# Performance work log

Hardware: AMD Instinct MI355X
Metric: run time of the kernel (lower is better)

The kernel has to match this reference:

```python
import jax, jax.numpy as jnp
import numpy as np

B, N, C = 2, 2048, 1024
H, D = 16, 64          # num_heads, head_dim
FF = 4096              # mlp hidden = 4*C
EPS = 1e-5


def layernorm(x, g, b):
    mu = jnp.mean(x, axis=-1, keepdims=True)
    var = jnp.mean((x - mu) ** 2, axis=-1, keepdims=True)
    return (x - mu) * jax.lax.rsqrt(var + EPS) * g + b


def setup_inputs() -> dict:
    key = jax.random.key(0)
    ks = jax.random.split(key, 8)
    s = lambda d: 1.0 / np.sqrt(d)
    return {
        "x": jax.random.normal(ks[0], (B, N, C), jnp.float32),
        "ln1_g": jnp.ones((C,), jnp.float32),
        "ln1_b": jnp.zeros((C,), jnp.float32),
        "qkv_w": jax.random.normal(ks[1], (3 * C, C), jnp.float32) * s(C),
        "proj_w": jax.random.normal(ks[2], (C, C), jnp.float32) * s(C),
        "proj_b": jnp.zeros((C,), jnp.float32),
        "ln2_g": jnp.ones((C,), jnp.float32),
        "ln2_b": jnp.zeros((C,), jnp.float32),
        "w1": jax.random.normal(ks[3], (FF, C), jnp.float32) * s(C),
        "b1": jnp.zeros((FF,), jnp.float32),
        "w2": jax.random.normal(ks[4], (C, FF), jnp.float32) * s(FF),
        "b2": jnp.zeros((C,), jnp.float32),
    }


def reference(x, ln1_g, ln1_b, qkv_w, proj_w, proj_b, ln2_g, ln2_b, w1, b1, w2, b2):
    # ---- attention sub-block ----
    h = layernorm(x, ln1_g, ln1_b)                       # [B,N,C]
    qkv = h @ qkv_w.T                                    # [B,N,3C]
    qkv = qkv.reshape(B, N, 3, H, D).transpose(2, 0, 3, 1, 4)  # [3,B,H,N,D]
    q, k, v = qkv[0], qkv[1], qkv[2]
    scale = D ** -0.5
    attn = jnp.einsum("bhnd,bhmd->bhnm", q, k) * scale   # [B,H,N,N]
    attn = jax.nn.softmax(attn, axis=-1)
    ao = jnp.einsum("bhnm,bhmd->bhnd", attn, v)          # [B,H,N,D]
    ao = ao.transpose(0, 2, 1, 3).reshape(B, N, C)
    x = x + ao @ proj_w.T + proj_b
    # ---- MLP sub-block ----
    h2 = layernorm(x, ln2_g, ln2_b)
    mlp = jax.nn.gelu(h2 @ w1.T + b1, approximate=False) @ w2.T + b2
    return x + mlp
```

## Files before the change

### kernel.cpp

```cpp
#include <hip/hip_runtime.h>
#include <hip/hip_bf16.h>

typedef __hip_bfloat16 obf;
typedef __attribute__((ext_vector_type(8))) __bf16 bf16x8;
typedef __attribute__((ext_vector_type(4))) float f32x4;

#define DEVINL __device__ __forceinline__

DEVINL void gload_lds16(const void* g, void* l) {
  __builtin_amdgcn_global_load_lds((const __attribute__((address_space(1))) void*)g,
                                   (__attribute__((address_space(3))) void*)l,
                                   16, 0, 0);
}

__global__ void __launch_bounds__(256) f2b_kernel(const float* __restrict__ in,
                                                  __bf16* __restrict__ out, int n8)
{
  const int i = blockIdx.x * 256 + threadIdx.x;
  if (i >= n8) return;
  const float4 a = ((const float4*)in)[i * 2];
  const float4 b = ((const float4*)in)[i * 2 + 1];
  bf16x8 o;
  o[0] = (__bf16)a.x; o[1] = (__bf16)a.y; o[2] = (__bf16)a.z; o[3] = (__bf16)a.w;
  o[4] = (__bf16)b.x; o[5] = (__bf16)b.y; o[6] = (__bf16)b.z; o[7] = (__bf16)b.w;
  ((bf16x8*)out)[i] = o;
}

__global__ void __launch_bounds__(256) ln_f2b2_kernel(
    const float* __restrict__ xin, const float* __restrict__ g, const float* __restrict__ b,
    obf* __restrict__ lnout,
    const float* __restrict__ win1, __bf16* __restrict__ wout1, int n8_1, int nb1,
    const float* __restrict__ win2, __bf16* __restrict__ wout2, int n8_2,
    int nln)
{
  __shared__ float red[8];
  const int t = threadIdx.x;
  const int bx = blockIdx.x;
  if (bx < nln) {
    const int row = bx;
    const int lane = t & 63, w = t >> 6;
    float4 f = ((const float4*)xin)[(size_t)row * 256 + t];
    float v[4] = { f.x, f.y, f.z, f.w };
    float s1 = v[0] + v[1] + v[2] + v[3];
    float s2 = v[0]*v[0] + v[1]*v[1] + v[2]*v[2] + v[3]*v[3];
    #pragma unroll
    for (int off = 32; off >= 1; off >>= 1) {
      s1 += __shfl_xor(s1, off);
      s2 += __shfl_xor(s2, off);
    }
    if (lane == 0) { red[w] = s1; red[4 + w] = s2; }
    __syncthreads();
    s1 = red[0] + red[1] + red[2] + red[3];
    s2 = red[4] + red[5] + red[6] + red[7];
    const float mu = s1 * (1.f / 1024.f);
    const float var = s2 * (1.f / 1024.f) - mu * mu;
    const float rs = rsqrtf(var + 1e-5f);
    const float4 gv = ((const float4*)g)[t];
    const float4 bv = ((const float4*)b)[t];
    obf* op = lnout + (size_t)row * 1024 + t * 4;
    op[0] = __float2bfloat16((v[0] - mu) * rs * gv.x + bv.x);
    op[1] = __float2bfloat16((v[1] - mu) * rs * gv.y + bv.y);
    op[2] = __float2bfloat16((v[2] - mu) * rs * gv.z + bv.z);
    op[3] = __float2bfloat16((v[3] - mu) * rs * gv.w + bv.w);
  } else if (bx < nln + nb1) {
    const int i = (bx - nln) * 256 + t;
    if (i >= n8_1) return;
    const float4 a = ((const float4*)win1)[i * 2];
    const float4 b2 = ((const float4*)win1)[i * 2 + 1];
    bf16x8 o;
    o[0] = (__bf16)a.x;  o[1] = (__bf16)a.y;  o[2] = (__bf16)a.z;  o[3] = (__bf16)a.w;
    o[4] = (__bf16)b2.x; o[5] = (__bf16)b2.y; o[6] = (__bf16)b2.z; o[7] = (__bf16)b2.w;
    ((bf16x8*)wout1)[i] = o;
  } else {
    const int i = (bx - nln - nb1) * 256 + t;
    if (i >= n8_2) return;
    const float4 a = ((const float4*)win2)[i * 2];
    const float4 b2 = ((const float4*)win2)[i * 2 + 1];
    bf16x8 o;
    o[0] = (__bf16)a.x;  o[1] = (__bf16)a.y;  o[2] = (__bf16)a.z;  o[3] = (__bf16)a.w;
    o[4] = (__bf16)b2.x; o[5] = (__bf16)b2.y; o[6] = (__bf16)b2.z; o[7] = (__bf16)b2.w;
    ((bf16x8*)wout2)[i] = o;
  }
}

enum { EPI_NONE = 0, EPI_BIAS_RES_F32OUT = 1, EPI_BIAS_GELU = 2, EPI_BIAS_RESF32_F32OUT = 3 };

template<int EPI, int NI>
__global__ void __launch_bounds__(256, 2) gemm_bt(
    const obf* __restrict__ A, const obf* __restrict__ Bw,
    void* __restrict__ Cout, const float* __restrict__ bias,
    const void* __restrict__ resid, int M, int N, int K)
{
  __shared__ __align__(16) char As[128 * 64 * 2];
  __shared__ __align__(16) char Bs[NI * 32 * 64 * 2];
  const int tid = threadIdx.x;
  const int lane = tid & 63;
  const int w = tid >> 6, wr = w >> 1, wc = w & 1;
  const int bm = blockIdx.y * 128, bn = blockIdx.x * (NI * 32);
  const size_t lda = (size_t)K * 2;

  f32x4 acc[4][NI];
  #pragma unroll
  for (int i = 0; i < 4; i++)
    #pragma unroll
    for (int j = 0; j < NI; j++) {
      acc[i][j][0] = 0.f; acc[i][j][1] = 0.f; acc[i][j][2] = 0.f; acc[i][j][3] = 0.f;
    }

  for (int k0 = 0; k0 < K; k0 += 64) {
    #pragma unroll
    for (int i = 0; i < 4; i++) {
      const int ci = tid + 256 * i;
      const int r = ci >> 3;
      const int gb = ((ci & 7) * 16) ^ ((r & 7) << 4);
      gload_lds16((const char*)A + (size_t)(bm + r) * lda + (size_t)k0 * 2 + gb, As + ci * 16);
    }
    #pragma unroll
    for (int i = 0; i < NI; i++) {
      const int ci = tid + 256 * i;
      const int r = ci >> 3;
      const int gb = ((ci & 7) * 16) ^ ((r & 7) << 4);
      gload_lds16((const char*)Bw + (size_t)(bn + r) * lda + (size_t)k0 * 2 + gb, Bs + ci * 16);
    }
    __syncthreads();

    bf16x8 af[4][2], bfr[NI][2];
    #pragma unroll
    for (int mi = 0; mi < 4; mi++) {
      const int r = wr * 64 + mi * 16 + (lane & 15);
      #pragma unroll
      for (int ks = 0; ks < 2; ks++) {
        const int cb = ks * 64 + ((lane >> 4) * 16);
        af[mi][ks] = *(const bf16x8*)(As + r * 128 + (cb ^ ((r & 7) << 4)));
      }
    }
    #pragma unroll
    for (int ni = 0; ni < NI; ni++) {
      const int r = wc * (NI * 16) + ni * 16 + (lane & 15);
      #pragma unroll
      for (int ks = 0; ks < 2; ks++) {
        const int cb = ks * 64 + ((lane >> 4) * 16);
        bfr[ni][ks] = *(const bf16x8*)(Bs + r * 128 + (cb ^ ((r & 7) << 4)));
      }
    }
    #pragma unroll
    for (int ks = 0; ks < 2; ks++)
      #pragma unroll
      for (int mi = 0; mi < 4; mi++)
        #pragma unroll
        for (int ni = 0; ni < NI; ni++)
          acc[mi][ni] = __builtin_amdgcn_mfma_f32_16x16x32_bf16(af[mi][ks], bfr[ni][ks], acc[mi][ni], 0, 0, 0);
    __syncthreads();
  }

  #pragma unroll
  for (int mi = 0; mi < 4; mi++) {
    #pragma unroll
    for (int ni = 0; ni < NI; ni++) {
      const int col = bn + wc * (NI * 16) + ni * 16 + (lane & 15);
      float bv = 0.f;
      if (EPI != EPI_NONE) bv = bias[col];
      #pragma unroll
      for (int r = 0; r < 4; r++) {
        const int row = bm + wr * 64 + mi * 16 + ((lane >> 4) << 2) + r;
        const float vacc = acc[mi][ni][r];
        const size_t idx = (size_t)row * N + col;
        if (EPI == EPI_NONE) {
          ((obf*)Cout)[idx] = __float2bfloat16(vacc);
        } else if (EPI == EPI_BIAS_RES_F32OUT) {
          const float x0 = ((const float*)resid)[idx];
          ((float*)Cout)[idx] = vacc + bv + x0;
        } else if (EPI == EPI_BIAS_GELU) {
          const float u = vacc + bv;
          const float e = exp2f(-2.30218709f * (u + 0.044715f * u * u * u));
          ((obf*)Cout)[idx] = __float2bfloat16(u / (1.f + e));
        } else {
          const float x0 = ((const float*)resid)[idx];
          ((float*)Cout)[idx] = vacc + bv + x0;
        }
      }
    }
  }
}

__global__ void __launch_bounds__(512, 2) attn_kernel(
    const obf* __restrict__ qkv_, obf* __restrict__ ao)
{
  const __bf16* qkv = (const __bf16*)qkv_;
  const int bid = blockIdx.x;
  const int xcd = bid & 7, idx = bid >> 3;
  const int bh = xcd * 4 + (idx >> 4);
  const int q0 = (idx & 15) * 128;
  const int b = bh >> 4, h = bh & 15;
  const int tid = threadIdx.x, lane = tid & 63, w = tid >> 6;
  const int l15 = lane & 15, hi = lane >> 4;

  __shared__ __align__(16) char Ks[2][64 * 128];
  __shared__ __align__(16) char Vs[2][64 * 128];
  __shared__ __align__(16) char Ps[8 * 16 * 128];

  bf16x8 qf[2];
  {
    const int qrow = q0 + w * 16 + l15;
    #pragma unroll
    for (int ks = 0; ks < 2; ks++)
      qf[ks] = *(const bf16x8*)(qkv + ((size_t)(b * 2048 + qrow)) * 3072 + h * 64 + ks * 32 + hi * 8);
  }

  f32x4 o[4];
  #pragma unroll
  for (int j = 0; j < 4; j++) { o[j][0]=0.f; o[j][1]=0.f; o[j][2]=0.f; o[j][3]=0.f; }
  float lrow[4] = { 0.f, 0.f, 0.f, 0.f };

  const float kfac = 0.125f * 1.44269504089f;

  const int kr = tid >> 3, kc = (tid & 7) * 8;
  const int kcb = (tid & 7) * 16;
  const int kswz = kcb ^ ((kr & 7) << 4);

  bf16x8 pk, pv;
  pk = *(const bf16x8*)(qkv + ((size_t)(b * 2048 + kr)) * 3072 + 1024 + h * 64 + kc);
  pv = *(const bf16x8*)(qkv + ((size_t)(b * 2048 + kr)) * 3072 + 2048 + h * 64 + kc);
  *(bf16x8*)(Ks[0] + kr * 128 + kswz) = pk;
  #pragma unroll
  for (int j = 0; j < 8; j++) {
    const int d = kc + j;
    *(__bf16*)(Vs[0] + d * 128 + ((kr * 2) ^ ((d & 7) << 4))) = pv[j];
  }
  __syncthreads();

  for (int kt = 0; kt < 2048; kt += 64) {
    const int cur = (kt >> 6) & 1;
    if (kt + 64 < 2048) {
      pk = *(const bf16x8*)(qkv + ((size_t)(b * 2048 + kt + 64 + kr)) * 3072 + 1024 + h * 64 + kc);
      pv = *(const bf16x8*)(qkv + ((size_t)(b * 2048 + kt + 64 + kr)) * 3072 + 2048 + h * 64 + kc);
    }

    f32x4 s[4];
    #pragma unroll
    for (int j = 0; j < 4; j++) { s[j][0]=0.f; s[j][1]=0.f; s[j][2]=0.f; s[j][3]=0.f; }
    #pragma unroll
    for (int ni = 0; ni < 4; ni++) {
      const int r = ni * 16 + l15;
      const bf16x8 kf0 = *(const bf16x8*)(Ks[cur] + r * 128 + ((hi * 16) ^ ((r & 7) << 4)));
      const bf16x8 kf1 = *(const bf16x8*)(Ks[cur] + r * 128 + ((64 + hi * 16) ^ ((r & 7) << 4)));
      s[ni] = __builtin_amdgcn_mfma_f32_16x16x32_bf16(qf[0], kf0, s[ni], 0, 0, 0);
      s[ni] = __builtin_amdgcn_mfma_f32_16x16x32_bf16(qf[1], kf1, s[ni], 0, 0, 0);
    }

    #pragma unroll
    for (int r = 0; r < 4; r++) {
      const int qrl = (hi << 2) + r;
      char* psrow = Ps + w * 2048 + qrl * 128;
      float psum = 0.f;
      #pragma unroll
      for (int ni = 0; ni < 4; ni++) {
        const float p = exp2f(s[ni][r] * kfac);
        psum += p;
        *(__bf16*)(psrow + (((ni * 16 + l15) * 2) ^ ((qrl & 7) << 4))) = (__bf16)p;
      }
      lrow[r] += psum;
    }

    #pragma unroll
    for (int ks = 0; ks < 2; ks++) {
      const int rr = l15;
      const bf16x8 pa = *(const bf16x8*)(Ps + w * 2048 + rr * 128 + (((ks * 32 + hi * 8) * 2) ^ ((rr & 7) << 4)));
      #pragma unroll
      for (int df = 0; df < 4; df++) {
        const int dr = df * 16 + l15;
        const int cb = (ks * 32 + hi * 8) * 2;
        const bf16x8 vb = *(const bf16x8*)(Vs[cur] + dr * 128 + (cb ^ ((dr & 7) << 4)));
        o[df] = __builtin_amdgcn_mfma_f32_16x16x32_bf16(pa, vb, o[df], 0, 0, 0);
      }
    }

    if (kt + 64 < 2048) {
      *(bf16x8*)(Ks[cur ^ 1] + kr * 128 + kswz) = pk;
      #pragma unroll
      for (int j = 0; j < 8; j++) {
        const int d = kc + j;
        *(__bf16*)(Vs[cur ^ 1] + d * 128 + ((kr * 2) ^ ((d & 7) << 4))) = pv[j];
      }
    }
    __syncthreads();
  }

  #pragma unroll
  for (int r = 0; r < 4; r++) {
    lrow[r] += __shfl_xor(lrow[r], 1);
    lrow[r] += __shfl_xor(lrow[r], 2);
    lrow[r] += __shfl_xor(lrow[r], 4);
    lrow[r] += __shfl_xor(lrow[r], 8);
  }
  #pragma unroll
  for (int r = 0; r < 4; r++) {
    const float inv = 1.f / lrow[r];
    const int qrow = q0 + w * 16 + (hi << 2) + r;
    #pragma unroll
    for (int df = 0; df < 4; df++) {
      const int col = h * 64 + df * 16 + l15;
      ao[((size_t)(b * 2048 + qrow)) * 1024 + col] = __float2bfloat16(o[df][r] * inv);
    }
  }
}

extern "C" void kernel_launch(void* const* d_in, const int* in_sizes, int n_in,
                              void* d_out, int out_size, void* d_ws, size_t ws_size,
                              hipStream_t stream) {
  const float* x      = (const float*)d_in[0];
  const float* ln1_g  = (const float*)d_in[1];
  const float* ln1_b  = (const float*)d_in[2];
  const float* qkv_w  = (const float*)d_in[3];
  const float* proj_w = (const float*)d_in[4];
  const float* proj_b = (const float*)d_in[5];
  const float* ln2_g  = (const float*)d_in[6];
  const float* ln2_b  = (const float*)d_in[7];
  const float* w1     = (const float*)d_in[8];
  const float* b1     = (const float*)d_in[9];
  const float* w2     = (const float*)d_in[10];
  const float* b2     = (const float*)d_in[11];
  float* out = (float*)d_out;

  char* ws = (char*)d_ws;
  float* x2   = (float*)ws;
  obf*   h    = (obf*)(ws + (16u << 20));
  obf*   qkv  = (obf*)(ws + (24u << 20));
  obf*   ao   = (obf*)(ws + (48u << 20));
  obf*   m1   = (obf*)(ws + (24u << 20));
  __bf16* wb_qkv  = (__bf16*)(ws + (56u << 20));
  __bf16* wb_proj = (__bf16*)(ws + (62u << 20));
  __bf16* wb_w1   = (__bf16*)(ws + (56u << 20));
  __bf16* wb_w2   = (__bf16*)(ws + (16u << 20));

  const int M = 4096;

  ln_f2b2_kernel<<<M + 1536 + 512, 256, 0, stream>>>(
      x, ln1_g, ln1_b, h,
      qkv_w, wb_qkv, 3072 * 1024 / 8, 1536,
      proj_w, wb_proj, 1024 * 1024 / 8, M);
  gemm_bt<EPI_NONE, 4><<<dim3(3072 / 128, M / 128), 256, 0, stream>>>(
      h, (const obf*)wb_qkv, qkv, nullptr, nullptr, M, 3072, 1024);
  attn_kernel<<<512, 512, 0, stream>>>(qkv, ao);
  gemm_bt<EPI_BIAS_RES_F32OUT, 2><<<dim3(1024 / 64, M / 128), 256, 0, stream>>>(
      ao, (const obf*)wb_proj, x2, proj_b, x, M, 1024, 1024);
  ln_f2b2_kernel<<<M + 2048, 256, 0, stream>>>(
      x2, ln2_g, ln2_b, h,
      w1, wb_w1, 4096 * 1024 / 8, 2048,
      nullptr, nullptr, 0, M);
  gemm_bt<EPI_BIAS_GELU, 4><<<dim3(4096 / 128, M / 128), 256, 0, stream>>>(
      h, (const obf*)wb_w1, m1, b1, nullptr, M, 4096, 1024);
  f2b_kernel<<<(4096 * 1024 / 8 + 255) / 256, 256, 0, stream>>>(w2, wb_w2, 4096 * 1024 / 8);
  gemm_bt<EPI_BIAS_RESF32_F32OUT, 2><<<dim3(1024 / 64, M / 128), 256, 0, stream>>>(
      m1, (const obf*)wb_w2, out, b2, x2, M, 1024, 4096);
}
```

Measured before the change: 250.3 us.

## Pre-transpose V, store residual x2 in bf16, fold w2 conversion into LN2

Adds a separate kernel that transposes V into a [bh][d][n] layout, so the attention kernel can write V tiles to LDS with one vector store instead of eight scalar scattered stores. The intermediate residual x2 is now kept in bf16 rather than fp32, which halves its write and its two later reads. The w2 fp32-to-bf16 conversion moves into the LN2 launch, removing one kernel launch. The cost is an extra transpose pass over V and extra rounding of the residual stream to bf16, which lowers accuracy.

New measurement: 233.8 us. -6.6%, faster.

```diff
diff --git a/kernel.cpp b/kernel.cpp
--- a/kernel.cpp
+++ b/kernel.cpp
@@ -13,21 +13,13 @@
                                    16, 0, 0);
 }
 
-__global__ void __launch_bounds__(256) f2b_kernel(const float* __restrict__ in,
-                                                  __bf16* __restrict__ out, int n8)
-{
-  const int i = blockIdx.x * 256 + threadIdx.x;
-  if (i >= n8) return;
-  const float4 a = ((const float4*)in)[i * 2];
-  const float4 b = ((const float4*)in)[i * 2 + 1];
-  bf16x8 o;
-  o[0] = (__bf16)a.x; o[1] = (__bf16)a.y; o[2] = (__bf16)a.z; o[3] = (__bf16)a.w;
-  o[4] = (__bf16)b.x; o[5] = (__bf16)b.y; o[6] = (__bf16)b.z; o[7] = (__bf16)b.w;
-  ((bf16x8*)out)[i] = o;
-}
-
+DEVINL float bf2f(unsigned short h) {
+  union { unsigned int u; float f; } c; c.u = ((unsigned)h) << 16; return c.f;
+}
+
+template<bool INBF16>
 __global__ void __launch_bounds__(256) ln_f2b2_kernel(
-    const float* __restrict__ xin, const float* __restrict__ g, const float* __restrict__ b,
+    const void* __restrict__ xin, const float* __restrict__ g, const float* __restrict__ b,
     obf* __restrict__ lnout,
     const float* __restrict__ win1, __bf16* __restrict__ wout1, int n8_1, int nb1,
     const float* __restrict__ win2, __bf16* __restrict__ wout2, int n8_2,
@@ -39,8 +31,14 @@
   if (bx < nln) {
     const int row = bx;
     const int lane = t & 63, w = t >> 6;
-    float4 f = ((const float4*)xin)[(size_t)row * 256 + t];
-    float v[4] = { f.x, f.y, f.z, f.w };
+    float v[4];
+    if (INBF16) {
+      ushort4 u = ((const ushort4*)xin)[(size_t)row * 256 + t];
+      v[0] = bf2f(u.x); v[1] = bf2f(u.y); v[2] = bf2f(u.z); v[3] = bf2f(u.w);
+    } else {
+      float4 f = ((const float4*)xin)[(size_t)row * 256 + t];
+      v[0] = f.x; v[1] = f.y; v[2] = f.z; v[3] = f.w;
+    }
     float s1 = v[0] + v[1] + v[2] + v[3];
     float s2 = v[0]*v[0] + v[1]*v[1] + v[2]*v[2] + v[3]*v[3];
     #pragma unroll
@@ -83,7 +81,7 @@
   }
 }
 
-enum { EPI_NONE = 0, EPI_BIAS_RES_F32OUT = 1, EPI_BIAS_GELU = 2, EPI_BIAS_RESF32_F32OUT = 3 };
+enum { EPI_NONE = 0, EPI_BIAS_RES_BF16OUT = 1, EPI_BIAS_GELU = 2, EPI_BIAS_RESBF16_F32OUT = 3 };
 
 template<int EPI, int NI>
 __global__ void __launch_bounds__(256, 2) gemm_bt(
@@ -167,15 +165,15 @@
         const size_t idx = (size_t)row * N + col;
         if (EPI == EPI_NONE) {
           ((obf*)Cout)[idx] = __float2bfloat16(vacc);
-        } else if (EPI == EPI_BIAS_RES_F32OUT) {
+        } else if (EPI == EPI_BIAS_RES_BF16OUT) {
           const float x0 = ((const float*)resid)[idx];
-          ((float*)Cout)[idx] = vacc + bv + x0;
+          ((obf*)Cout)[idx] = __float2bfloat16(vacc + bv + x0);
         } else if (EPI == EPI_BIAS_GELU) {
           const float u = vacc + bv;
           const float e = exp2f(-2.30218709f * (u + 0.044715f * u * u * u));
           ((obf*)Cout)[idx] = __float2bfloat16(u / (1.f + e));
         } else {
-          const float x0 = ((const float*)resid)[idx];
+          const float x0 = __bfloat162float(((const obf*)resid)[idx]);
           ((float*)Cout)[idx] = vacc + bv + x0;
         }
       }
@@ -183,10 +181,40 @@
   }
 }
 
+__global__ void __launch_bounds__(256) vtrans_kernel(const obf* __restrict__ qkv, obf* __restrict__ vt)
+{
+  const int bh = blockIdx.y;
+  const int b = bh >> 4, h = bh & 15;
+  const int n0 = blockIdx.x * 64;
+  __shared__ __bf16 tile[64][72];
+  const int t = threadIdx.x;
+  {
+    const int n = t >> 2;
+    const int c0 = (t & 3) * 16;
+    const __bf16* src = (const __bf16*)qkv + ((size_t)(b * 2048 + n0 + n)) * 3072 + 2048 + h * 64 + c0;
+    bf16x8 u0 = *(const bf16x8*)src;
+    bf16x8 u1 = *(const bf16x8*)(src + 8);
+    #pragma unroll
+    for (int j = 0; j < 8; j++) { tile[n][c0 + j] = u0[j]; tile[n][c0 + 8 + j] = u1[j]; }
+  }
+  __syncthreads();
+  {
+    const int d = t >> 2;
+    const int c0 = (t & 3) * 16;
+    bf16x8 o0, o1;
+    #pragma unroll
+    for (int j = 0; j < 8; j++) { o0[j] = tile[c0 + j][d]; o1[j] = tile[c0 + 8 + j][d]; }
+    __bf16* dst = (__bf16*)vt + ((size_t)bh * 64 + d) * 2048 + n0 + c0;
+    *(bf16x8*)dst = o0;
+    *(bf16x8*)(dst + 8) = o1;
+  }
+}
+
 __global__ void __launch_bounds__(512, 2) attn_kernel(
-    const obf* __restrict__ qkv_, obf* __restrict__ ao)
+    const obf* __restrict__ qkv_, const obf* __restrict__ vt_, obf* __restrict__ ao)
 {
   const __bf16* qkv = (const __bf16*)qkv_;
+  const __bf16* vt  = (const __bf16*)vt_;
   const int bid = blockIdx.x;
   const int xcd = bid & 7, idx = bid >> 3;
   const int bh = xcd * 4 + (idx >> 4);
@@ -220,20 +248,16 @@
 
   bf16x8 pk, pv;
   pk = *(const bf16x8*)(qkv + ((size_t)(b * 2048 + kr)) * 3072 + 1024 + h * 64 + kc);
-  pv = *(const bf16x8*)(qkv + ((size_t)(b * 2048 + kr)) * 3072 + 2048 + h * 64 + kc);
+  pv = *(const bf16x8*)(vt + ((size_t)bh * 64 + kr) * 2048 + kc);
   *(bf16x8*)(Ks[0] + kr * 128 + kswz) = pk;
-  #pragma unroll
-  for (int j = 0; j < 8; j++) {
-    const int d = kc + j;
-    *(__bf16*)(Vs[0] + d * 128 + ((kr * 2) ^ ((d & 7) << 4))) = pv[j];
-  }
+  *(bf16x8*)(Vs[0] + kr * 128 + kswz) = pv;
   __syncthreads();
 
   for (int kt = 0; kt < 2048; kt += 64) {
     const int cur = (kt >> 6) & 1;
     if (kt + 64 < 2048) {
       pk = *(const bf16x8*)(qkv + ((size_t)(b * 2048 + kt + 64 + kr)) * 3072 + 1024 + h * 64 + kc);
-      pv = *(const bf16x8*)(qkv + ((size_t)(b * 2048 + kt + 64 + kr)) * 3072 + 2048 + h * 64 + kc);
+      pv = *(const bf16x8*)(vt + ((size_t)bh * 64 + kr) * 2048 + kt + 64 + kc);
     }
 
     f32x4 s[4];
@@ -277,11 +301,7 @@
 
     if (kt + 64 < 2048) {
       *(bf16x8*)(Ks[cur ^ 1] + kr * 128 + kswz) = pk;
-      #pragma unroll
-      for (int j = 0; j < 8; j++) {
-        const int d = kc + j;
-        *(__bf16*)(Vs[cur ^ 1] + d * 128 + ((kr * 2) ^ ((d & 7) << 4))) = pv[j];
-      }
+      *(bf16x8*)(Vs[cur ^ 1] + kr * 128 + kswz) = pv;
     }
     __syncthreads();
   }
@@ -323,34 +343,35 @@
   float* out = (float*)d_out;
 
   char* ws = (char*)d_ws;
-  float* x2   = (float*)ws;
-  obf*   h    = (obf*)(ws + (16u << 20));
-  obf*   qkv  = (obf*)(ws + (24u << 20));
-  obf*   ao   = (obf*)(ws + (48u << 20));
-  obf*   m1   = (obf*)(ws + (24u << 20));
+  obf*   x2      = (obf*)ws;
+  obf*   vt      = (obf*)(ws + ( 8u << 20));
+  __bf16* wb_w2  = (__bf16*)(ws + ( 8u << 20));
+  obf*   h       = (obf*)(ws + (16u << 20));
+  obf*   qkv     = (obf*)(ws + (24u << 20));
+  obf*   ao      = (obf*)(ws + (48u << 20));
+  obf*   m1      = (obf*)(ws + (24u << 20));
   __bf16* wb_qkv  = (__bf16*)(ws + (56u << 20));
   __bf16* wb_proj = (__bf16*)(ws + (62u << 20));
   __bf16* wb_w1   = (__bf16*)(ws + (56u << 20));
-  __bf16* wb_w2   = (__bf16*)(ws + (16u << 20));
 
   const int M = 4096;
 
-  ln_f2b2_kernel<<<M + 1536 + 512, 256, 0, stream>>>(
+  ln_f2b2_kernel<false><<<M + 1536 + 512, 256, 0, stream>>>(
       x, ln1_g, ln1_b, h,
       qkv_w, wb_qkv, 3072 * 1024 / 8, 1536,
       proj_w, wb_proj, 1024 * 1024 / 8, M);
   gemm_bt<EPI_NONE, 4><<<dim3(3072 / 128, M / 128), 256, 0, stream>>>(
       h, (const obf*)wb_qkv, qkv, nullptr, nullptr, M, 3072, 1024);
-  attn_kernel<<<512, 512, 0, stream>>>(qkv, ao);
-  gemm_bt<EPI_BIAS_RES_F32OUT, 2><<<dim3(1024 / 64, M / 128), 256, 0, stream>>>(
+  vtrans_kernel<<<dim3(32, 32), 256, 0, stream>>>(qkv, vt);
+  attn_kernel<<<512, 512, 0, stream>>>(qkv, vt, ao);
+  gemm_bt<EPI_BIAS_RES_BF16OUT, 2><<<dim3(1024 / 64, M / 128), 256, 0, stream>>>(
       ao, (const obf*)wb_proj, x2, proj_b, x, M, 1024, 1024);
-  ln_f2b2_kernel<<<M + 2048, 256, 0, stream>>>(
+  ln_f2b2_kernel<true><<<M + 2048 + 2048, 256, 0, stream>>>(
       x2, ln2_g, ln2_b, h,
       w1, wb_w1, 4096 * 1024 / 8, 2048,
-      nullptr, nullptr, 0, M);
+      w2, wb_w2, 4096 * 1024 / 8, M);
   gemm_bt<EPI_BIAS_GELU, 4><<<dim3(4096 / 128, M / 128), 256, 0, stream>>>(
       h, (const obf*)wb_w1, m1, b1, nullptr, M, 4096, 1024);
-  f2b_kernel<<<(4096 * 1024 / 8 + 255) / 256, 256, 0, stream>>>(w2, wb_w2, 4096 * 1024 / 8);
-  gemm_bt<EPI_BIAS_RESF32_F32OUT, 2><<<dim3(1024 / 64, M / 128), 256, 0, stream>>>(
+  gemm_bt<EPI_BIAS_RESBF16_F32OUT, 2><<<dim3(1024 / 64, M / 128), 256, 0, stream>>>(
       m1, (const obf*)wb_w2, out, b2, x2, M, 1024, 4096);
 }
```
